# Kernel tuning notes

Measured on AMD Instinct MI355X. Metric: run time of the kernel, lower is better.

The kernel has to match this reference:

```python
import jax, jax.numpy as jnp
import numpy as np

C = 64
C2 = C // 2

def setup_inputs() -> dict:
    key = jax.random.key(0)
    ks = jax.random.split(key, 5)
    x = jax.random.normal(ks[0], (8, C, 64, 64), dtype=jnp.float32)
    # 1x1 conv weights stored as [out, in] matrices (kernel size 1)
    g_w = jax.random.normal(ks[1], (C2, C), dtype=jnp.float32) * (1.0 / np.sqrt(C))
    g_b = jax.random.normal(ks[2], (C2,), dtype=jnp.float32) * 0.01
    W_w = jax.random.normal(ks[3], (C, C2), dtype=jnp.float32) * (1.0 / np.sqrt(C2))
    W_b = jax.random.normal(ks[4], (C,), dtype=jnp.float32) * 0.01
    return {"x": x, "g_w": g_w, "g_b": g_b, "W_w": W_w, "W_b": W_b}

def reference(x, g_w, g_b, W_w, W_b):
    b, c, h, w = x.shape
    xf = x.reshape(b, c, h * w)                      # [B, C, N]
    # g: 1x1 conv -> [B, N, C2]
    g_x = jnp.einsum('oc,bcn->bno', g_w, xf) + g_b
    # attention scores on raw x (theta/phi convs unused in original forward)
    f = jnp.einsum('bcn,bcm->bnm', xf, xf)           # [B, N, N]
    f_div_C = jax.nn.softmax(f, axis=-1)
    y = jnp.einsum('bnm,bmo->bno', f_div_C, g_x)     # [B, N, C2]
    # W: 1x1 conv back to C channels, then residual
    W_y = jnp.einsum('co,bno->bcn', W_w, y) + W_b[None, :, None]
    z = W_y.reshape(b, c, h, w) + x
    return z
```

## Files before the change

kernel.cpp:

```cpp
#include <hip/hip_runtime.h>
#include <hip/hip_bf16.h>

#define BATCH 8
#define CH    64
#define CH2   32
#define NN    4096
#define BN    (BATCH * NN)
#define KPAD  72
#define YPAD  36
#define RPAD  40

typedef __attribute__((ext_vector_type(8)))  short        short8;
typedef __attribute__((ext_vector_type(4)))  float        floatx4;
typedef __attribute__((ext_vector_type(16))) float        floatx16;
typedef __attribute__((ext_vector_type(4)))  unsigned int uint4v;
typedef __attribute__((ext_vector_type(8)))  unsigned short ushort8v;
typedef unsigned short ushort_t;

#define LOG2E 1.4426950408889634f

__device__ __forceinline__ unsigned short f2bf_rne(float f) {
    unsigned int u = __float_as_uint(f);
    return (unsigned short)((u + 0x7FFFu + ((u >> 16) & 1u)) >> 16);
}

__global__ __launch_bounds__(256) void prep_fused(const float* __restrict__ x,
                                                  const float* __restrict__ gw,
                                                  const float* __restrict__ gb,
                                                  ushort_t* __restrict__ xT,
                                                  float* __restrict__ mlog,
                                                  ushort_t* __restrict__ gxT) {
    __shared__ float gwl[CH2 * CH];
    __shared__ float gbl[CH2];
    int t = threadIdx.x;
    for (int i = t; i < CH2 * CH; i += 256) gwl[i] = gw[i];
    if (t < CH2) gbl[t] = gb[t];
    __syncthreads();

    int g   = blockIdx.x * 256 + t;
    int row = g >> 2;
    int q4  = g & 3;
    int b = row >> 12, n = row & (NN - 1);
    const float* xp = x + (size_t)b * CH * NN + n;

    float xv[16];
    float ns = 0.f;
    short8 v0, v1;
    #pragma unroll
    for (int j = 0; j < 8; ++j) {
        float a = xp[(size_t)(q4 * 16 + j) * NN];
        xv[j] = a; ns += a * a;
        v0[j] = (short)f2bf_rne(a);
    }
    #pragma unroll
    for (int j = 0; j < 8; ++j) {
        float a = xp[(size_t)(q4 * 16 + 8 + j) * NN];
        xv[8 + j] = a; ns += a * a;
        v1[j] = (short)f2bf_rne(a);
    }
    *(short8*)(xT + (size_t)row * CH + q4 * 16)     = v0;
    *(short8*)(xT + (size_t)row * CH + q4 * 16 + 8) = v1;
    ns += __shfl_xor(ns, 1);
    ns += __shfl_xor(ns, 2);
    if (q4 == 0) mlog[row] = 12.0f * sqrtf(ns) * LOG2E;

    float acc[CH2];
    #pragma unroll
    for (int o = 0; o < CH2; ++o) acc[o] = 0.f;
    #pragma unroll
    for (int j = 0; j < 16; ++j) {
        float a = xv[j];
        const float* gc = gwl + q4 * 16 + j;
        #pragma unroll
        for (int o = 0; o < CH2; ++o) acc[o] = fmaf(gc[o * CH], a, acc[o]);
    }
    #pragma unroll
    for (int o = 0; o < CH2; ++o) {
        acc[o] += __shfl_xor(acc[o], 1);
        acc[o] += __shfl_xor(acc[o], 2);
    }
    #pragma unroll
    for (int i = 0; i < 8; ++i) {
        int o = q4 * 8 + i;
        gxT[((size_t)b * CH2 + o) * NN + n] = f2bf_rne(acc[o] + gbl[o]);
    }
}

__global__ __launch_bounds__(256, 4) void flash_attn(const ushort_t* __restrict__ xT,
                                                     const ushort_t* __restrict__ gxT,
                                                     const float* __restrict__ mlog,
                                                     ushort_t* __restrict__ py,
                                                     float* __restrict__ pl,
                                                     int ksplit) {
    __shared__ ushort_t Klds[64 * KPAD];
    __shared__ float    Ybuf[4][32 * YPAD];

    const int tid = threadIdx.x, wave = tid >> 6, lane = tid & 63;
    const int q5 = lane & 31;
    const int h  = lane >> 5;
    const int bq = blockIdx.x & 255;
    const int sp = blockIdx.x >> 8;
    const int b = bq >> 5, qt = bq & 31;
    const int n0 = qt * 128 + wave * 32;
    const int k0 = sp * ksplit;

    short8 qf[4];
    {
        const ushort_t* qp = xT + ((size_t)(b * NN + n0 + q5)) * CH + h * 8;
        #pragma unroll
        for (int f = 0; f < 4; ++f) qf[f] = *(const short8*)(qp + f * 16);
    }
    const float ml = mlog[(size_t)b * NN + n0 + q5];

    floatx16 yt;
    #pragma unroll
    for (int i = 0; i < 16; ++i) yt[i] = 0.f;
    float rs = 0.f;

    const ushort_t* kb = xT + (size_t)(b * NN + k0) * CH;
    const ushort_t* vb = gxT + (size_t)b * CH2 * NN + k0;
    const int iters = ksplit >> 6;
    const int skey = tid >> 3, sc0 = (tid & 7) * 8;

    for (int kt = 0; kt < iters; ++kt) {
        short8 kv0 = *(const short8*)(kb + ((size_t)kt << 12) + (size_t)skey * CH + sc0);
        short8 kv1 = *(const short8*)(kb + ((size_t)kt << 12) + (size_t)(skey + 32) * CH + sc0);
        short8 vf[4];
        #pragma unroll
        for (int fr = 0; fr < 4; ++fr)
            vf[fr] = *(const short8*)(vb + (size_t)q5 * NN + kt * 64 + fr * 16 + h * 8);

        __syncthreads();
        *(short8*)(&Klds[skey * KPAD + sc0])        = kv0;
        *(short8*)(&Klds[(skey + 32) * KPAD + sc0]) = kv1;
        __syncthreads();

        #pragma unroll
        for (int T = 0; T < 2; ++T) {
            floatx16 st;
            #pragma unroll
            for (int i = 0; i < 16; ++i) st[i] = 0.f;
            #pragma unroll
            for (int f = 0; f < 4; ++f) {
                short8 kf = *(const short8*)(&Klds[(T * 32 + q5) * KPAD + f * 16 + h * 8]);
                st = __builtin_amdgcn_mfma_f32_32x32x16_bf16(kf, qf[f], st, 0, 0, 0);
            }
            unsigned int d[8];
            #pragma unroll
            for (int r2 = 0; r2 < 8; ++r2) {
                float p0 = __builtin_amdgcn_exp2f(fmaf(st[2 * r2],     LOG2E, -ml));
                float p1 = __builtin_amdgcn_exp2f(fmaf(st[2 * r2 + 1], LOG2E, -ml));
                rs += p0; rs += p1;
                d[r2] = ((__float_as_uint(p0) + 0x8000u) >> 16) |
                        ((__float_as_uint(p1) + 0x8000u) & 0xFFFF0000u);
            }
            #pragma unroll
            for (int fp = 0; fp < 2; ++fp) {
                unsigned int d0 = d[fp * 4 + 0], d1 = d[fp * 4 + 1];
                unsigned int d2 = d[fp * 4 + 2], d3 = d[fp * 4 + 3];
                unsigned int e0 = (unsigned int)__shfl_xor((int)d0, 32);
                unsigned int e1 = (unsigned int)__shfl_xor((int)d1, 32);
                unsigned int e2 = (unsigned int)__shfl_xor((int)d2, 32);
                unsigned int e3 = (unsigned int)__shfl_xor((int)d3, 32);
                uint4v bv;
                bv[0] = h ? e2 : d0;
                bv[1] = h ? e3 : d1;
                bv[2] = h ? d2 : e0;
                bv[3] = h ? d3 : e1;
                short8 pb = __builtin_bit_cast(short8, bv);
                yt = __builtin_amdgcn_mfma_f32_32x32x16_bf16(vf[T * 2 + fp], pb, yt, 0, 0, 0);
            }
        }
    }

    rs += __shfl_xor(rs, 32);
    float* yb = Ybuf[wave];
    #pragma unroll
    for (int reg = 0; reg < 16; ++reg) {
        int o = (reg & 3) + 8 * (reg >> 2) + 4 * h;
        yb[q5 * YPAD + o] = yt[reg];
    }
    __syncthreads();
    {
        int qq = lane >> 1, half = lane & 1;
        const float* src = yb + qq * YPAD + half * 16;
        float4 s0 = *(const float4*)(src);
        float4 s1 = *(const float4*)(src + 4);
        float4 s2 = *(const float4*)(src + 8);
        float4 s3 = *(const float4*)(src + 12);
        ushort8v pk0, pk1;
        pk0[0] = f2bf_rne(s0.x); pk0[1] = f2bf_rne(s0.y);
        pk0[2] = f2bf_rne(s0.z); pk0[3] = f2bf_rne(s0.w);
        pk0[4] = f2bf_rne(s1.x); pk0[5] = f2bf_rne(s1.y);
        pk0[6] = f2bf_rne(s1.z); pk0[7] = f2bf_rne(s1.w);
        pk1[0] = f2bf_rne(s2.x); pk1[1] = f2bf_rne(s2.y);
        pk1[2] = f2bf_rne(s2.z); pk1[3] = f2bf_rne(s2.w);
        pk1[4] = f2bf_rne(s3.x); pk1[5] = f2bf_rne(s3.y);
        pk1[6] = f2bf_rne(s3.z); pk1[7] = f2bf_rne(s3.w);
        ushort_t* dst = py + ((size_t)sp * BN + (size_t)b * NN + n0 + qq) * CH2 + half * 16;
        *(ushort8v*)(dst)     = pk0;
        *(ushort8v*)(dst + 8) = pk1;
    }
    if (h == 0) pl[(size_t)sp * BN + (size_t)b * NN + n0 + q5] = rs;
}

__global__ __launch_bounds__(256) void reduce_proj(const ushort_t* __restrict__ py,
                                                   const float* __restrict__ pl,
                                                   const float* __restrict__ Ww,
                                                   const float* __restrict__ Wb,
                                                   const float* __restrict__ x,
                                                   float* __restrict__ out,
                                                   int nsplit) {
    __shared__ ushort_t WwB[CH * RPAD];
    __shared__ ushort_t Y[64 * RPAD];
    __shared__ float    linv[64];
    __shared__ float    WbL[CH];

    const int t = threadIdx.x;
    const int row = t >> 2, o8 = (t & 3) * 8;
    const int grow0 = blockIdx.x * 64;

    {
        const float* wp = Ww + row * CH2 + o8;
        ushort8v w;
        #pragma unroll
        for (int j = 0; j < 8; ++j) w[j] = f2bf_rne(wp[j]);
        *(ushort8v*)(&WwB[row * RPAD + o8]) = w;
    }
    if (t < CH) WbL[t] = Wb[t];
    if (t < 64) {
        float l = 0.f;
        for (int s = 0; s < nsplit; ++s) l += pl[(size_t)s * BN + grow0 + t];
        linv[t] = 1.0f / l;
    }

    float acc[8];
    #pragma unroll
    for (int j = 0; j < 8; ++j) acc[j] = 0.f;
    for (int s = 0; s < nsplit; ++s) {
        ushort8v v = *(const ushort8v*)(py + ((size_t)s * BN + grow0 + row) * CH2 + o8);
        #pragma unroll
        for (int j = 0; j < 8; ++j)
            acc[j] += __uint_as_float((unsigned int)v[j] << 16);
    }
    __syncthreads();
    {
        float inv = linv[row];
        ushort8v yv;
        #pragma unroll
        for (int j = 0; j < 8; ++j) yv[j] = f2bf_rne(acc[j] * inv);
        *(ushort8v*)(&Y[row * RPAD + o8]) = yv;
    }
    __syncthreads();

    const int wave = t >> 6, lane = t & 63;
    const int ql = lane & 15, quad = lane >> 4;
    const int b = grow0 >> 12;
    const int nbase = (grow0 & (NN - 1)) + wave * 16;

    short8 bfrag = *(const short8*)(&Y[(wave * 16 + ql) * RPAD + quad * 8]);
    #pragma unroll
    for (int ct = 0; ct < 4; ++ct) {
        short8 afrag = *(const short8*)(&WwB[(ct * 16 + ql) * RPAD + quad * 8]);
        floatx4 d = (floatx4){0.f, 0.f, 0.f, 0.f};
        d = __builtin_amdgcn_mfma_f32_16x16x32_bf16(afrag, bfrag, d, 0, 0, 0);
        #pragma unroll
        for (int r = 0; r < 4; ++r) {
            int c = ct * 16 + quad * 4 + r;
            size_t oi = ((size_t)b * CH + c) * NN + nbase + ql;
            out[oi] = d[r] + WbL[c] + x[oi];
        }
    }
}

extern "C" void kernel_launch(void* const* d_in, const int* in_sizes, int n_in,
                              void* d_out, int out_size, void* d_ws, size_t ws_size,
                              hipStream_t stream) {
    const float* x  = (const float*)d_in[0];
    const float* gw = (const float*)d_in[1];
    const float* gb = (const float*)d_in[2];
    const float* Ww = (const float*)d_in[3];
    const float* Wb = (const float*)d_in[4];
    float* out = (float*)d_out;

    ushort_t* xT   = (ushort_t*)d_ws;
    ushort_t* gxT  = xT + (size_t)BN * CH;
    float*    mlog = (float*)(gxT + (size_t)BATCH * CH2 * NN);
    ushort_t* py   = (ushort_t*)(mlog + BN);
    size_t base_bytes = (size_t)BN * CH * 2 + (size_t)BATCH * CH2 * NN * 2 + (size_t)BN * 4;
    int split = 4;
    while (split > 1 && base_bytes + (size_t)split * BN * (CH2 * 2 + 4) > ws_size)
        split >>= 1;
    float* pl = (float*)(py + (size_t)split * BN * CH2);

    hipLaunchKernelGGL(prep_fused,  dim3(BN * 4 / 256), dim3(256), 0, stream,
                       x, gw, gb, xT, mlog, gxT);
    hipLaunchKernelGGL(flash_attn,  dim3(256 * split),  dim3(256), 0, stream,
                       xT, gxT, mlog, py, pl, NN / split);
    hipLaunchKernelGGL(reduce_proj, dim3(BN / 64),      dim3(256), 0, stream,
                       py, pl, Ww, Wb, x, out, split);
}
```

Before: 126.6 us.

## Fold log2e into bf16 keys, seed scores with -max, compute row sums via MFMA

Pre-scales x by sqrt(log2e) before the bf16 conversion so QK scores come out already in the log2 domain, and seeds the MFMA accumulator with -ml, which removes the per-element FMA before exp2. The per-lane row-sum accumulation is replaced by an extra MFMA against a vector of bf16 ones, so the sum uses the same rounded probabilities as the PV product and the VALU adds go away. The bf16 packing uses a byte permute, and the K tile and Y staging buffer now share one LDS allocation, which needs an added barrier before reuse. The extra MFMA per block raises matrix-unit work, and the sqrt(log2e) scaling alters the bf16 rounding of the keys.

```diff
diff --git a/kernel.cpp b/kernel.cpp
--- a/kernel.cpp
+++ b/kernel.cpp
@@ -17,7 +17,8 @@
 typedef __attribute__((ext_vector_type(8)))  unsigned short ushort8v;
 typedef unsigned short ushort_t;
 
-#define LOG2E 1.4426950408889634f
+#define LOG2E      1.4426950408889634f
+#define SQRT_LOG2E 1.2011224087864498f
 
 __device__ __forceinline__ unsigned short f2bf_rne(float f) {
     unsigned int u = __float_as_uint(f);
@@ -50,13 +51,13 @@
     for (int j = 0; j < 8; ++j) {
         float a = xp[(size_t)(q4 * 16 + j) * NN];
         xv[j] = a; ns += a * a;
-        v0[j] = (short)f2bf_rne(a);
+        v0[j] = (short)f2bf_rne(a * SQRT_LOG2E);
     }
     #pragma unroll
     for (int j = 0; j < 8; ++j) {
         float a = xp[(size_t)(q4 * 16 + 8 + j) * NN];
         xv[8 + j] = a; ns += a * a;
-        v1[j] = (short)f2bf_rne(a);
+        v1[j] = (short)f2bf_rne(a * SQRT_LOG2E);
     }
     *(short8*)(xT + (size_t)row * CH + q4 * 16)     = v0;
     *(short8*)(xT + (size_t)row * CH + q4 * 16 + 8) = v1;
@@ -92,8 +93,8 @@
                                                      ushort_t* __restrict__ py,
                                                      float* __restrict__ pl,
                                                      int ksplit) {
-    __shared__ ushort_t Klds[64 * KPAD];
-    __shared__ float    Ybuf[4][32 * YPAD];
+    __shared__ __align__(16) unsigned char smem[4 * 32 * YPAD * 4];
+    ushort_t* Klds = (ushort_t*)smem;
 
     const int tid = threadIdx.x, wave = tid >> 6, lane = tid & 63;
     const int q5 = lane & 31;
@@ -112,10 +113,13 @@
     }
     const float ml = mlog[(size_t)b * NN + n0 + q5];
 
-    floatx16 yt;
-    #pragma unroll
-    for (int i = 0; i < 16; ++i) yt[i] = 0.f;
-    float rs = 0.f;
+    short8 ones;
+    #pragma unroll
+    for (int j = 0; j < 8; ++j) ones[j] = (short)0x3F80;
+
+    floatx16 yt, lt;
+    #pragma unroll
+    for (int i = 0; i < 16; ++i) { yt[i] = 0.f; lt[i] = 0.f; }
 
     const ushort_t* kb = xT + (size_t)(b * NN + k0) * CH;
     const ushort_t* vb = gxT + (size_t)b * CH2 * NN + k0;
@@ -139,7 +143,7 @@
         for (int T = 0; T < 2; ++T) {
             floatx16 st;
             #pragma unroll
-            for (int i = 0; i < 16; ++i) st[i] = 0.f;
+            for (int i = 0; i < 16; ++i) st[i] = -ml;
             #pragma unroll
             for (int f = 0; f < 4; ++f) {
                 short8 kf = *(const short8*)(&Klds[(T * 32 + q5) * KPAD + f * 16 + h * 8]);
@@ -148,11 +152,11 @@
             unsigned int d[8];
             #pragma unroll
             for (int r2 = 0; r2 < 8; ++r2) {
-                float p0 = __builtin_amdgcn_exp2f(fmaf(st[2 * r2],     LOG2E, -ml));
-                float p1 = __builtin_amdgcn_exp2f(fmaf(st[2 * r2 + 1], LOG2E, -ml));
-                rs += p0; rs += p1;
-                d[r2] = ((__float_as_uint(p0) + 0x8000u) >> 16) |
-                        ((__float_as_uint(p1) + 0x8000u) & 0xFFFF0000u);
+                float p0 = __builtin_amdgcn_exp2f(st[2 * r2]);
+                float p1 = __builtin_amdgcn_exp2f(st[2 * r2 + 1]);
+                unsigned int u0 = __float_as_uint(p0) + 0x8000u;
+                unsigned int u1 = __float_as_uint(p1) + 0x8000u;
+                d[r2] = __builtin_amdgcn_perm(u1, u0, 0x07060302u);
             }
             #pragma unroll
             for (int fp = 0; fp < 2; ++fp) {
@@ -169,12 +173,13 @@
                 bv[3] = h ? d3 : e1;
                 short8 pb = __builtin_bit_cast(short8, bv);
                 yt = __builtin_amdgcn_mfma_f32_32x32x16_bf16(vf[T * 2 + fp], pb, yt, 0, 0, 0);
+                lt = __builtin_amdgcn_mfma_f32_32x32x16_bf16(ones, pb, lt, 0, 0, 0);
             }
         }
     }
 
-    rs += __shfl_xor(rs, 32);
-    float* yb = Ybuf[wave];
+    __syncthreads();
+    float* yb = (float*)smem + wave * 32 * YPAD;
     #pragma unroll
     for (int reg = 0; reg < 16; ++reg) {
         int o = (reg & 3) + 8 * (reg >> 2) + 4 * h;
@@ -201,7 +206,7 @@
         *(ushort8v*)(dst)     = pk0;
         *(ushort8v*)(dst + 8) = pk1;
     }
-    if (h == 0) pl[(size_t)sp * BN + (size_t)b * NN + n0 + q5] = rs;
+    if (h == 0) pl[(size_t)sp * BN + (size_t)b * NN + n0 + q5] = lt[0];
 }
 
 __global__ __launch_bounds__(256) void reduce_proj(const ushort_t* __restrict__ py,
```

Result: faster. 123.2 us (median of 2 runs) (-2.7%).
